# Performance work log

Measured on AMD Instinct MI355X. Metric: run time of the kernel, lower is better.

## Reference

```python
import jax, jax.numpy as jnp
import numpy as np

B, N, IN_F, OUT_F = 32, 1024, 256, 256
ALPHA = 0.2  # LeakyReLU negative slope
NEG_INF = -9e15  # matches torch's -9000000000000000.0 masking constant


def setup_inputs() -> dict:
    key = jax.random.key(0)
    k1, k2, k3, k4 = jax.random.split(key, 4)
    h = jax.random.normal(k1, (B, N, IN_F), dtype=jnp.float32)
    adj = jax.random.randint(k2, (B, N, N), 0, 2, dtype=jnp.int32)
    W = jax.random.normal(k3, (OUT_F, IN_F), dtype=jnp.float32) * 0.05
    a = jax.random.normal(k4, (1, 2 * OUT_F), dtype=jnp.float32) * 0.05
    return {"h": h, "adj": adj, "W": W, "a": a}


def reference(h, adj, W, a):
    # Wh: (B, N, out)
    Wh = jnp.einsum("bni,oi->bno", h, W)
    # Decompose a([Wh_i || Wh_j]) = Wh_i . a1 + Wh_j . a2 (identical math,
    # avoids the O(B*N^2*2*out) concat intermediate of the torch code).
    a1 = a[0, :OUT_F]   # (out,)
    a2 = a[0, OUT_F:]   # (out,)
    si = Wh @ a1        # (B, N) score contribution of source node i
    sj = Wh @ a2        # (B, N) score contribution of neighbor node j
    e = jax.nn.leaky_relu(si[:, :, None] + sj[:, None, :], negative_slope=ALPHA)
    attention = jnp.where(adj > 0, e, NEG_INF)
    attention = jax.nn.softmax(attention, axis=-1)
    # dropout omitted (eval mode)
    h_prime = jnp.einsum("bij,bjo->bio", attention, Wh)
    return jax.nn.elu(h_prime)
```

## Files before the change

### kernel.cpp

```cpp
#include <hip/hip_runtime.h>
#include <hip/hip_bf16.h>


#define ALPHA 0.2f
#define LOG2E 1.44269504f

typedef __bf16 bf16x8 __attribute__((ext_vector_type(8)));
typedef __bf16 bf16x4 __attribute__((ext_vector_type(4)));
typedef float  f32x4  __attribute__((ext_vector_type(4)));
typedef unsigned long long u64;

__global__ __launch_bounds__(256) void k0_mask(const int* __restrict__ adj,
                                               u64* __restrict__ maskT) {
    const int wid = (blockIdx.x * 256 + threadIdx.x) >> 6;
    const int l   = threadIdx.x & 63;
    const size_t base = (size_t)wid * 64;
    #pragma unroll 4
    for (int it = 0; it < 64; ++it) {
        const size_t word = base + it;
        const int b  = (int)(word >> 14);
        const int jc = (int)((word >> 10) & 15);
        const int i  = (int)(word & 1023);
        const int v  = adj[(((size_t)b << 10) + i) * 1024 + jc * 64 + l];
        const u64 m  = __ballot(v > 0);
        if (l == 0) maskT[word] = m;
    }
}

__global__ __launch_bounds__(256) void k1_gemm1(const float* __restrict__ h,
                                                const float* __restrict__ W,
                                                const float* __restrict__ a_g,
                                                __bf16* __restrict__ whT,
                                                float* __restrict__ si,
                                                float* __restrict__ sj) {
    __shared__ __bf16 hA[64 * 72];
    __shared__ __bf16 hB[256 * 72];
    __shared__ float  red[512];
    const int t    = threadIdx.x;
    const int r0   = blockIdx.x * 64;
    const int b    = r0 >> 10;
    const int n0   = r0 & 1023;
    const int w    = t >> 6;
    const int l    = t & 63;
    const int ln   = l & 15;
    const int quad = l >> 4;

    f32x4 acc[4][4] = {};
    float4 ha_r[4], wb_r[16];

    #pragma unroll
    for (int it = 0; it < 4; ++it)
        ha_r[it] = *(const float4*)&h[(size_t)(r0 + it * 16 + (t >> 4)) * 256 + (t & 15) * 4];
    #pragma unroll
    for (int it = 0; it < 16; ++it)
        wb_r[it] = *(const float4*)&W[(size_t)(it * 16 + (t >> 4)) * 256 + (t & 15) * 4];

    for (int kc = 0; kc < 4; ++kc) {
        #pragma unroll
        for (int it = 0; it < 4; ++it) {
            const float4 v = ha_r[it];
            bf16x4 pv = {(__bf16)v.x, (__bf16)v.y, (__bf16)v.z, (__bf16)v.w};
            *(bf16x4*)&hA[(it * 16 + (t >> 4)) * 72 + (t & 15) * 4] = pv;
        }
        #pragma unroll
        for (int it = 0; it < 16; ++it) {
            const float4 v = wb_r[it];
            bf16x4 pv = {(__bf16)v.x, (__bf16)v.y, (__bf16)v.z, (__bf16)v.w};
            *(bf16x4*)&hB[(it * 16 + (t >> 4)) * 72 + (t & 15) * 4] = pv;
        }
        __syncthreads();
        if (kc < 3) {
            const int k0 = (kc + 1) * 64;
            #pragma unroll
            for (int it = 0; it < 4; ++it)
                ha_r[it] = *(const float4*)&h[(size_t)(r0 + it * 16 + (t >> 4)) * 256 + k0 + (t & 15) * 4];
            #pragma unroll
            for (int it = 0; it < 16; ++it)
                wb_r[it] = *(const float4*)&W[(size_t)(it * 16 + (t >> 4)) * 256 + k0 + (t & 15) * 4];
        }
        #pragma unroll
        for (int kk = 0; kk < 2; ++kk) {
            bf16x8 af[4], bfr[4];
            #pragma unroll
            for (int ri = 0; ri < 4; ++ri)
                af[ri] = *(const bf16x8*)&hA[(ri * 16 + ln) * 72 + kk * 32 + quad * 8];
            #pragma unroll
            for (int oi = 0; oi < 4; ++oi)
                bfr[oi] = *(const bf16x8*)&hB[(w * 64 + oi * 16 + ln) * 72 + kk * 32 + quad * 8];
            #pragma unroll
            for (int ri = 0; ri < 4; ++ri)
                #pragma unroll
                for (int oi = 0; oi < 4; ++oi)
                    acc[ri][oi] = __builtin_amdgcn_mfma_f32_16x16x32_bf16(
                        af[ri], bfr[oi], acc[ri][oi], 0, 0, 0);
        }
        __syncthreads();
    }

    #pragma unroll
    for (int ri = 0; ri < 4; ++ri) {
        const int n = ri * 16 + quad * 4;
        #pragma unroll
        for (int oi = 0; oi < 4; ++oi) {
            const int o = w * 64 + oi * 16 + ln;
            bf16x4 pv = {(__bf16)acc[ri][oi][0], (__bf16)acc[ri][oi][1],
                         (__bf16)acc[ri][oi][2], (__bf16)acc[ri][oi][3]};
            *(bf16x4*)&hB[o * 72 + n] = pv;
        }
    }
    __syncthreads();

    #pragma unroll
    for (int it = 0; it < 8; ++it) {
        const int o   = w * 64 + it * 8 + (l >> 3);
        const int seg = l & 7;
        const bf16x8 v = *(const bf16x8*)&hB[o * 72 + seg * 8];
        *(bf16x8*)&whT[((size_t)b * 256 + o) * 1024 + n0 + seg * 8] = v;
    }

    {
        float s1 = 0.f, s2 = 0.f;
        #pragma unroll 8
        for (int oi = 0; oi < 64; ++oi) {
            const int o = w * 64 + oi;
            const float v = (float)hB[o * 72 + l];
            s1 += v * a_g[o];
            s2 += v * a_g[256 + o];
        }
        red[w * 64 + l]       = s1;
        red[256 + w * 64 + l] = s2;
    }
    __syncthreads();
    if (t < 64) {
        si[b * 1024 + n0 + t] =
            (red[t] + red[64 + t] + red[128 + t] + red[192 + t]) * LOG2E;
    } else if (t < 128) {
        const int n = t - 64;
        sj[b * 1024 + n0 + n] =
            (red[256 + n] + red[320 + n] + red[384 + n] + red[448 + n]) * LOG2E;
    }
}

#define K3_BODY(JC, MC, SJC, MN, SJN)                                          \
  {                                                                            \
    const int j0 = (JC) * 64;                                                  \
     \
    _Pragma("unroll")                                                          \
    for (int it = 0; it < 8; ++it)                                             \
      *(bf16x8*)&lds_w[(it * 32 + (t >> 3)) * 72 + (t & 7) * 8] = vreg[it];    \
              \
    if ((JC) < 15) {                                                           \
      _Pragma("unroll")                                                        \
      for (int it = 0; it < 8; ++it)                                           \
        vreg[it] = *(const bf16x8*)&whTb[                                      \
            (size_t)(it * 32 + (t >> 3)) * 1024 + j0 + 64 + (t & 7) * 8];      \
      _Pragma("unroll")                                                        \
      for (int m = 0; m < 4; ++m)                                              \
        MN[m] = maskTb[(size_t)((JC) + 1) * 1024 + i0 + m * 16 + g];           \
      SJN = *(const float4*)&sj_g[bs + j0 + 64 + j4 * 4];                      \
    }                                                                          \
         \
    _Pragma("unroll")                                                          \
    for (int m = 0; m < 4; ++m) {                                              \
      const int il = m * 16 + g;                                               \
      const unsigned bits = (unsigned)(MC[m] >> (4 * j4)) & 0xFu;              \
      float e0 = si_r[m] + SJC.x; e0 = fmaxf(e0, ALPHA * e0);                  \
      float e1 = si_r[m] + SJC.y; e1 = fmaxf(e1, ALPHA * e1);                  \
      float e2 = si_r[m] + SJC.z; e2 = fmaxf(e2, ALPHA * e2);                  \
      float e3 = si_r[m] + SJC.w; e3 = fmaxf(e3, ALPHA * e3);                  \
      const float w0 = (bits & 1u) ? exp2f(e0) : 0.f;                          \
      const float w1 = (bits & 2u) ? exp2f(e1) : 0.f;                          \
      const float w2 = (bits & 4u) ? exp2f(e2) : 0.f;                          \
      const float w3 = (bits & 8u) ? exp2f(e3) : 0.f;                          \
      bf16x4 pv = {(__bf16)w0, (__bf16)w1, (__bf16)w2, (__bf16)w3};            \
      dsum[m] += (float)pv[0] + (float)pv[1] + (float)pv[2] + (float)pv[3];    \
      *(bf16x4*)&lds_s[il * 72 + j4 * 4] = pv;                                 \
    }                                                                          \
                       \
    asm volatile("s_waitcnt lgkmcnt(0)");                                      \
    __builtin_amdgcn_s_barrier();                                              \
                                                    \
    __builtin_amdgcn_s_setprio(1);                                             \
    _Pragma("unroll")                                                          \
    for (int kk = 0; kk < 2; ++kk) {                                           \
      bf16x8 af[4], bfr[4];                                                    \
      _Pragma("unroll")                                                        \
      for (int ri = 0; ri < 4; ++ri)                                           \
        af[ri] = *(const bf16x8*)&lds_s[(ri * 16 + ln) * 72 + kk * 32 + quad * 8]; \
      _Pragma("unroll")                                                        \
      for (int oi = 0; oi < 4; ++oi)                                           \
        bfr[oi] = *(const bf16x8*)&lds_w[(w * 64 + oi * 16 + ln) * 72 + kk * 32 + quad * 8]; \
      _Pragma("unroll")                                                        \
      for (int ri = 0; ri < 4; ++ri)                                           \
        _Pragma("unroll")                                                      \
        for (int oi = 0; oi < 4; ++oi)                                         \
          acc[ri][oi] = __builtin_amdgcn_mfma_f32_16x16x32_bf16(               \
              af[ri], bfr[oi], acc[ri][oi], 0, 0, 0);                          \
    }                                                                          \
    __builtin_amdgcn_s_setprio(0);                                             \
     \
                                \
    asm volatile("s_waitcnt lgkmcnt(0)");                                      \
    __builtin_amdgcn_s_barrier();                                              \
  }

__global__ __launch_bounds__(256, 2) void k3_attn(const u64* __restrict__ maskT,
                                                  const __bf16* __restrict__ whT,
                                                  const float* __restrict__ si_g,
                                                  const float* __restrict__ sj_g,
                                                  float* __restrict__ out) {
    __shared__ __bf16 lds_w[256 * 72];
    __shared__ __bf16 lds_s[64 * 72];
    __shared__ float  lds_denom[64];
    const int t = threadIdx.x;
    const int orig = blockIdx.x;
    const int wgid = (orig & 7) * 64 + (orig >> 3);
    const int b    = wgid >> 4;
    const int i0   = (wgid & 15) << 6;
    const int w    = t >> 6;
    const int l    = t & 63;
    const int ln   = l & 15;
    const int quad = l >> 4;
    const int g    = t >> 4;
    const int j4   = t & 15;
    const int bs   = b * 1024;

    float si_r[4];
    #pragma unroll
    for (int m = 0; m < 4; ++m) si_r[m] = si_g[bs + i0 + m * 16 + g];

    float dsum[4] = {0.f, 0.f, 0.f, 0.f};
    f32x4 acc[4][4] = {};
    const __bf16* whTb   = whT + (size_t)b * 256 * 1024;
    const u64*    maskTb = maskT + (size_t)b * 16384;

    bf16x8 vreg[8];
    u64    m_c[4], m_n[4];
    float4 sj_c, sj_n;

    #pragma unroll
    for (int it = 0; it < 8; ++it)
        vreg[it] = *(const bf16x8*)&whTb[(size_t)(it * 32 + (t >> 3)) * 1024 + (t & 7) * 8];
    #pragma unroll
    for (int m = 0; m < 4; ++m) m_c[m] = maskTb[i0 + m * 16 + g];
    sj_c = *(const float4*)&sj_g[bs + j4 * 4];

    for (int jj = 0; jj < 8; ++jj) {
        K3_BODY(2 * jj,     m_c, sj_c, m_n, sj_n);
        K3_BODY(2 * jj + 1, m_n, sj_n, m_c, sj_c);
    }

    #pragma unroll
    for (int m = 0; m < 4; ++m) {
        float v = dsum[m];
        v += __shfl_xor(v, 1);
        v += __shfl_xor(v, 2);
        v += __shfl_xor(v, 4);
        v += __shfl_xor(v, 8);
        if (j4 == 0) lds_denom[m * 16 + g] = v;
    }
    __syncthreads();
    #pragma unroll
    for (int ri = 0; ri < 4; ++ri) {
        #pragma unroll
        for (int q = 0; q < 4; ++q) {
            const int il = ri * 16 + quad * 4 + q;
            const float dinv = 1.0f / fmaxf(lds_denom[il], 1e-30f);
            #pragma unroll
            for (int oi = 0; oi < 4; ++oi) {
                const int o = w * 64 + oi * 16 + ln;
                const float v = acc[ri][oi][q] * dinv;
                const float r = v > 0.f ? v : __expf(v) - 1.f;
                out[((size_t)(bs + i0 + il)) * 256 + o] = r;
            }
        }
    }
}

extern "C" void kernel_launch(void* const* d_in, const int* in_sizes, int n_in,
                              void* d_out, int out_size, void* d_ws, size_t ws_size,
                              hipStream_t stream) {
    const float* h   = (const float*)d_in[0];
    const int*   adj = (const int*)d_in[1];
    const float* W   = (const float*)d_in[2];
    const float* a   = (const float*)d_in[3];
    float* out = (float*)d_out;

    __bf16* whT   = (__bf16*)d_ws;
    float*  si    = (float*)((char*)d_ws + (size_t)16777216);
    float*  sj    = (float*)((char*)d_ws + (size_t)16777216 + 131072);
    u64*    maskT = (u64*)((char*)d_ws + (size_t)16777216 + 262144);

    k0_mask<<<2048, 256, 0, stream>>>(adj, maskT);
    k1_gemm1<<<512, 256, 0, stream>>>(h, W, a, whT, si, sj);
    k3_attn<<<512, 256, 0, stream>>>(maskT, whT, si, sj, out);
}
```

Baseline: 285.0 us.

## Fuse adjacency masking into attention kernel and widen to 512-thread blocks

Removes the separate kernel that packed the int32 adjacency matrix into bitmasks. The attention kernel now reads adjacency rows directly as int4 vectors, prefetched one chunk ahead alongside the Wh and sj data. Blocks grow to 512 threads (8 waves), each wave covering 32 output columns, and each thread computes scores for two rows. This saves a launch and the bitmask write and re-read, but the streaming adjacency read now sits inside the attention kernel and adds register pressure there.

```diff
diff --git a/kernel.cpp b/kernel.cpp
--- a/kernel.cpp
+++ b/kernel.cpp
@@ -9,23 +9,6 @@
 typedef __bf16 bf16x4 __attribute__((ext_vector_type(4)));
 typedef float  f32x4  __attribute__((ext_vector_type(4)));
 typedef unsigned long long u64;
-
-__global__ __launch_bounds__(256) void k0_mask(const int* __restrict__ adj,
-                                               u64* __restrict__ maskT) {
-    const int wid = (blockIdx.x * 256 + threadIdx.x) >> 6;
-    const int l   = threadIdx.x & 63;
-    const size_t base = (size_t)wid * 64;
-    #pragma unroll 4
-    for (int it = 0; it < 64; ++it) {
-        const size_t word = base + it;
-        const int b  = (int)(word >> 14);
-        const int jc = (int)((word >> 10) & 15);
-        const int i  = (int)(word & 1023);
-        const int v  = adj[(((size_t)b << 10) + i) * 1024 + jc * 64 + l];
-        const u64 m  = __ballot(v > 0);
-        if (l == 0) maskT[word] = m;
-    }
-}
 
 __global__ __launch_bounds__(256) void k1_gemm1(const float* __restrict__ h,
                                                 const float* __restrict__ W,
@@ -141,70 +124,74 @@
     }
 }
 
-#define K3_BODY(JC, MC, SJC, MN, SJN)                                          \
+#define K3_BODY(JC, A0C, A1C, SJC, A0N, A1N, SJN)                              \
   {                                                                            \
     const int j0 = (JC) * 64;                                                  \
-     \
+       \
     _Pragma("unroll")                                                          \
-    for (int it = 0; it < 8; ++it)                                             \
-      *(bf16x8*)&lds_w[(it * 32 + (t >> 3)) * 72 + (t & 7) * 8] = vreg[it];    \
+    for (int it = 0; it < 4; ++it)                                             \
+      *(bf16x8*)&lds_w[(it * 64 + (t >> 3)) * 72 + (t & 7) * 8] = vreg[it];    \
               \
     if ((JC) < 15) {                                                           \
       _Pragma("unroll")                                                        \
-      for (int it = 0; it < 8; ++it)                                           \
+      for (int it = 0; it < 4; ++it)                                           \
         vreg[it] = *(const bf16x8*)&whTb[                                      \
-            (size_t)(it * 32 + (t >> 3)) * 1024 + j0 + 64 + (t & 7) * 8];      \
-      _Pragma("unroll")                                                        \
-      for (int m = 0; m < 4; ++m)                                              \
-        MN[m] = maskTb[(size_t)((JC) + 1) * 1024 + i0 + m * 16 + g];           \
+            (size_t)(it * 64 + (t >> 3)) * 1024 + j0 + 64 + (t & 7) * 8];      \
+      A0N = *(const int4*)&adjb[(size_t)rowg * 1024 + j0 + 64 + j4 * 4];       \
+      A1N = *(const int4*)&adjb[(size_t)(rowg + 32) * 1024 + j0 + 64 + j4 * 4];\
       SJN = *(const float4*)&sj_g[bs + j0 + 64 + j4 * 4];                      \
     }                                                                          \
          \
-    _Pragma("unroll")                                                          \
-    for (int m = 0; m < 4; ++m) {                                              \
-      const int il = m * 16 + g;                                               \
-      const unsigned bits = (unsigned)(MC[m] >> (4 * j4)) & 0xFu;              \
-      float e0 = si_r[m] + SJC.x; e0 = fmaxf(e0, ALPHA * e0);                  \
-      float e1 = si_r[m] + SJC.y; e1 = fmaxf(e1, ALPHA * e1);                  \
-      float e2 = si_r[m] + SJC.z; e2 = fmaxf(e2, ALPHA * e2);                  \
-      float e3 = si_r[m] + SJC.w; e3 = fmaxf(e3, ALPHA * e3);                  \
-      const float w0 = (bits & 1u) ? exp2f(e0) : 0.f;                          \
-      const float w1 = (bits & 2u) ? exp2f(e1) : 0.f;                          \
-      const float w2 = (bits & 4u) ? exp2f(e2) : 0.f;                          \
-      const float w3 = (bits & 8u) ? exp2f(e3) : 0.f;                          \
+    {                                                                          \
+      float e0 = si0 + SJC.x; e0 = fmaxf(e0, ALPHA * e0);                      \
+      float e1 = si0 + SJC.y; e1 = fmaxf(e1, ALPHA * e1);                      \
+      float e2 = si0 + SJC.z; e2 = fmaxf(e2, ALPHA * e2);                      \
+      float e3 = si0 + SJC.w; e3 = fmaxf(e3, ALPHA * e3);                      \
+      const float w0 = A0C.x > 0 ? exp2f(e0) : 0.f;                            \
+      const float w1 = A0C.y > 0 ? exp2f(e1) : 0.f;                            \
+      const float w2 = A0C.z > 0 ? exp2f(e2) : 0.f;                            \
+      const float w3 = A0C.w > 0 ? exp2f(e3) : 0.f;                            \
       bf16x4 pv = {(__bf16)w0, (__bf16)w1, (__bf16)w2, (__bf16)w3};            \
-      dsum[m] += (float)pv[0] + (float)pv[1] + (float)pv[2] + (float)pv[3];    \
-      *(bf16x4*)&lds_s[il * 72 + j4 * 4] = pv;                                 \
-    }                                                                          \
-                       \
-    asm volatile("s_waitcnt lgkmcnt(0)");                                      \
-    __builtin_amdgcn_s_barrier();                                              \
-                                                    \
+      dsum0 += (float)pv[0] + (float)pv[1] + (float)pv[2] + (float)pv[3];      \
+      *(bf16x4*)&lds_s[rowg * 72 + j4 * 4] = pv;                               \
+    }                                                                          \
+    {                                                                          \
+      float e0 = si1 + SJC.x; e0 = fmaxf(e0, ALPHA * e0);                      \
+      float e1 = si1 + SJC.y; e1 = fmaxf(e1, ALPHA * e1);                      \
+      float e2 = si1 + SJC.z; e2 = fmaxf(e2, ALPHA * e2);                      \
+      float e3 = si1 + SJC.w; e3 = fmaxf(e3, ALPHA * e3);                      \
+      const float w0 = A1C.x > 0 ? exp2f(e0) : 0.f;                            \
+      const float w1 = A1C.y > 0 ? exp2f(e1) : 0.f;                            \
+      const float w2 = A1C.z > 0 ? exp2f(e2) : 0.f;                            \
+      const float w3 = A1C.w > 0 ? exp2f(e3) : 0.f;                            \
+      bf16x4 pv = {(__bf16)w0, (__bf16)w1, (__bf16)w2, (__bf16)w3};            \
+      dsum1 += (float)pv[0] + (float)pv[1] + (float)pv[2] + (float)pv[3];      \
+      *(bf16x4*)&lds_s[(rowg + 32) * 72 + j4 * 4] = pv;                        \
+    }                                                                          \
+    __syncthreads();                                                           \
+                                \
     __builtin_amdgcn_s_setprio(1);                                             \
     _Pragma("unroll")                                                          \
     for (int kk = 0; kk < 2; ++kk) {                                           \
-      bf16x8 af[4], bfr[4];                                                    \
+      bf16x8 af[4], bfr[2];                                                    \
       _Pragma("unroll")                                                        \
       for (int ri = 0; ri < 4; ++ri)                                           \
         af[ri] = *(const bf16x8*)&lds_s[(ri * 16 + ln) * 72 + kk * 32 + quad * 8]; \
       _Pragma("unroll")                                                        \
-      for (int oi = 0; oi < 4; ++oi)                                           \
-        bfr[oi] = *(const bf16x8*)&lds_w[(w * 64 + oi * 16 + ln) * 72 + kk * 32 + quad * 8]; \
+      for (int oi = 0; oi < 2; ++oi)                                           \
+        bfr[oi] = *(const bf16x8*)&lds_w[(w * 32 + oi * 16 + ln) * 72 + kk * 32 + quad * 8]; \
       _Pragma("unroll")                                                        \
       for (int ri = 0; ri < 4; ++ri)                                           \
         _Pragma("unroll")                                                      \
-        for (int oi = 0; oi < 4; ++oi)                                         \
+        for (int oi = 0; oi < 2; ++oi)                                         \
           acc[ri][oi] = __builtin_amdgcn_mfma_f32_16x16x32_bf16(               \
               af[ri], bfr[oi], acc[ri][oi], 0, 0, 0);                          \
     }                                                                          \
     __builtin_amdgcn_s_setprio(0);                                             \
-     \
-                                \
-    asm volatile("s_waitcnt lgkmcnt(0)");                                      \
-    __builtin_amdgcn_s_barrier();                                              \
+    __syncthreads();                                                           \
   }
 
-__global__ __launch_bounds__(256, 2) void k3_attn(const u64* __restrict__ maskT,
+__global__ __launch_bounds__(512, 4) void k3_attn(const int* __restrict__ adj,
                                                   const __bf16* __restrict__ whT,
                                                   const float* __restrict__ si_g,
                                                   const float* __restrict__ sj_g,
@@ -221,43 +208,47 @@
     const int l    = t & 63;
     const int ln   = l & 15;
     const int quad = l >> 4;
-    const int g    = t >> 4;
+    const int rowg = t >> 4;
     const int j4   = t & 15;
     const int bs   = b * 1024;
 
-    float si_r[4];
-    #pragma unroll
-    for (int m = 0; m < 4; ++m) si_r[m] = si_g[bs + i0 + m * 16 + g];
-
-    float dsum[4] = {0.f, 0.f, 0.f, 0.f};
-    f32x4 acc[4][4] = {};
-    const __bf16* whTb   = whT + (size_t)b * 256 * 1024;
-    const u64*    maskTb = maskT + (size_t)b * 16384;
-
-    bf16x8 vreg[8];
-    u64    m_c[4], m_n[4];
+    const float si0 = si_g[bs + i0 + rowg];
+    const float si1 = si_g[bs + i0 + rowg + 32];
+
+    float dsum0 = 0.f, dsum1 = 0.f;
+    f32x4 acc[4][2] = {};
+    const __bf16* whTb = whT + (size_t)b * 256 * 1024;
+    const int*    adjb = adj + ((size_t)(bs + i0)) * 1024;
+
+    bf16x8 vreg[4];
+    int4   a0_c, a1_c, a0_n, a1_n;
     float4 sj_c, sj_n;
 
     #pragma unroll
-    for (int it = 0; it < 8; ++it)
-        vreg[it] = *(const bf16x8*)&whTb[(size_t)(it * 32 + (t >> 3)) * 1024 + (t & 7) * 8];
-    #pragma unroll
-    for (int m = 0; m < 4; ++m) m_c[m] = maskTb[i0 + m * 16 + g];
+    for (int it = 0; it < 4; ++it)
+        vreg[it] = *(const bf16x8*)&whTb[(size_t)(it * 64 + (t >> 3)) * 1024 + (t & 7) * 8];
+    a0_c = *(const int4*)&adjb[(size_t)rowg * 1024 + j4 * 4];
+    a1_c = *(const int4*)&adjb[(size_t)(rowg + 32) * 1024 + j4 * 4];
     sj_c = *(const float4*)&sj_g[bs + j4 * 4];
 
     for (int jj = 0; jj < 8; ++jj) {
-        K3_BODY(2 * jj,     m_c, sj_c, m_n, sj_n);
-        K3_BODY(2 * jj + 1, m_n, sj_n, m_c, sj_c);
-    }
-
-    #pragma unroll
-    for (int m = 0; m < 4; ++m) {
-        float v = dsum[m];
+        K3_BODY(2 * jj,     a0_c, a1_c, sj_c, a0_n, a1_n, sj_n);
+        K3_BODY(2 * jj + 1, a0_n, a1_n, sj_n, a0_c, a1_c, sj_c);
+    }
+
+    {
+        float v = dsum0;
         v += __shfl_xor(v, 1);
         v += __shfl_xor(v, 2);
         v += __shfl_xor(v, 4);
         v += __shfl_xor(v, 8);
-        if (j4 == 0) lds_denom[m * 16 + g] = v;
+        if (j4 == 0) lds_denom[rowg] = v;
+        float u = dsum1;
+        u += __shfl_xor(u, 1);
+        u += __shfl_xor(u, 2);
+        u += __shfl_xor(u, 4);
+        u += __shfl_xor(u, 8);
+        if (j4 == 0) lds_denom[rowg + 32] = u;
     }
     __syncthreads();
     #pragma unroll
@@ -267,8 +258,8 @@
             const int il = ri * 16 + quad * 4 + q;
             const float dinv = 1.0f / fmaxf(lds_denom[il], 1e-30f);
             #pragma unroll
-            for (int oi = 0; oi < 4; ++oi) {
-                const int o = w * 64 + oi * 16 + ln;
+            for (int oi = 0; oi < 2; ++oi) {
+                const int o = w * 32 + oi * 16 + ln;
                 const float v = acc[ri][oi][q] * dinv;
                 const float r = v > 0.f ? v : __expf(v) - 1.f;
                 out[((size_t)(bs + i0 + il)) * 256 + o] = r;
@@ -286,12 +277,10 @@
     const float* a   = (const float*)d_in[3];
     float* out = (float*)d_out;
 
-    __bf16* whT   = (__bf16*)d_ws;
-    float*  si    = (float*)((char*)d_ws + (size_t)16777216);
-    float*  sj    = (float*)((char*)d_ws + (size_t)16777216 + 131072);
-    u64*    maskT = (u64*)((char*)d_ws + (size_t)16777216 + 262144);
-
-    k0_mask<<<2048, 256, 0, stream>>>(adj, maskT);
+    __bf16* whT = (__bf16*)d_ws;
+    float*  si  = (float*)((char*)d_ws + (size_t)16777216);
+    float*  sj  = (float*)((char*)d_ws + (size_t)16777216 + 131072);
+
     k1_gemm1<<<512, 256, 0, stream>>>(h, W, a, whT, si, sj);
-    k3_attn<<<512, 256, 0, stream>>>(maskT, whT, si, sj, out);
+    k3_attn<<<512, 512, 0, stream>>>(adj, whT, si, sj, out);
 }
```

Result: faster. 250.4 us (-12.1%).
